# Optimization experiments

Hardware: AMD Instinct MI355X
Metric: run time of the kernel (lower is better)

Reference implementation:

```python
import jax, jax.numpy as jnp
import numpy as np

D_MODEL = 1024
N_HEADS = 16
D_K = D_MODEL // N_HEADS
B, S = 2, 2048


def setup_inputs() -> dict:
    key = jax.random.key(0)
    ks = jax.random.split(key, 11)
    s = 1.0 / np.sqrt(D_MODEL)
    return {
        "q": jax.random.normal(ks[0], (B, S, D_MODEL), jnp.float32),
        "k": jax.random.normal(ks[1], (B, S, D_MODEL), jnp.float32),
        "v": jax.random.normal(ks[2], (B, S, D_MODEL), jnp.float32),
        "Wq": jax.random.normal(ks[3], (D_MODEL, D_MODEL), jnp.float32) * s,
        "bq": jnp.zeros((D_MODEL,), jnp.float32),
        "Wk": jax.random.normal(ks[4], (D_MODEL, D_MODEL), jnp.float32) * s,
        "bk": jnp.zeros((D_MODEL,), jnp.float32),
        "Wv": jax.random.normal(ks[5], (D_MODEL, D_MODEL), jnp.float32) * s,
        "bv": jnp.zeros((D_MODEL,), jnp.float32),
        "Wo": jax.random.normal(ks[6], (D_MODEL, D_MODEL), jnp.float32) * s,
        "bo": jnp.zeros((D_MODEL,), jnp.float32),
    }


def reference(q, k, v, Wq, bq, Wk, bk, Wv, bv, Wo, bo):
    b = q.shape[0]
    # linear projections then split heads: [b, s, d] -> [b, h, s, d_k]
    def proj(x, W, bias):
        y = jnp.einsum('bsd,ed->bse', x, W) + bias  # torch Linear: x @ W.T + b
        return y.reshape(b, -1, N_HEADS, D_K).transpose(0, 2, 1, 3)

    qh, kh, vh = proj(q, Wq, bq), proj(k, Wk, bk), proj(v, Wv, bv)
    scores = jnp.einsum('bhqd,bhkd->bhqk', qh, kh) / np.sqrt(D_K)
    attn = jax.nn.softmax(scores, axis=-1)  # dropout: identity (eval mode)
    x = jnp.einsum('bhqk,bhkd->bhqd', attn, vh)
    x = x.transpose(0, 2, 1, 3).reshape(b, -1, D_MODEL)
    return jnp.einsum('bsd,ed->bse', x, Wo) + bo
```

## Files before the change

kernel.cpp:

```cpp
#include <hip/hip_runtime.h>
#include <math.h>
#include <stdint.h>

#define DM 1024
#define NH 16
#define DKH 64
#define BB 2
#define SS 2048
#define MM (BB*SS)

typedef __bf16 bf16;
typedef __bf16 bf16x8 __attribute__((ext_vector_type(8)));
typedef __bf16 bf16x4 __attribute__((ext_vector_type(4)));
typedef float f32x4 __attribute__((ext_vector_type(4)));

#define MFMA16(a,b,c) __builtin_amdgcn_mfma_f32_16x16x32_bf16((a),(b),(c),0,0,0)

#define SOFTMAX_C 12.0f
#define QSCALE 0.1803368801111204f

__device__ static inline void g2l16(const void* g, void* l) {
  __builtin_amdgcn_global_load_lds(
      (const __attribute__((address_space(1))) unsigned int*)g,
      (__attribute__((address_space(3))) unsigned int*)l, 16, 0, 0);
}

__global__ __launch_bounds__(256) void cvt_all(
    const float* __restrict__ q, const float* __restrict__ k, const float* __restrict__ v,
    const float* __restrict__ wq, const float* __restrict__ wk,
    const float* __restrict__ wv, const float* __restrict__ wo,
    bf16* __restrict__ Xq, bf16* __restrict__ Xk, bf16* __restrict__ Xv,
    bf16* __restrict__ Wqb, bf16* __restrict__ Wkb, bf16* __restrict__ Wvb,
    bf16* __restrict__ Wob)
{
  const long i = (long)blockIdx.x * 256 + threadIdx.x;
  const float* src; bf16* dst; long off;
  if (i < 3L * 524288L) {
    const int a = (int)(i / 524288L);
    off = (i % 524288L) * 8;
    src = (a == 0) ? q : (a == 1) ? k : v;
    dst = (a == 0) ? Xq : (a == 1) ? Xk : Xv;
  } else {
    const long j = i - 3L * 524288L;
    const int a = (int)(j / 131072L);
    off = (j % 131072L) * 8;
    src = (a == 0) ? wq : (a == 1) ? wk : (a == 2) ? wv : wo;
    dst = (a == 0) ? Wqb : (a == 1) ? Wkb : (a == 2) ? Wvb : Wob;
  }
  float4 f0 = *(const float4*)(src + off);
  float4 f1 = *(const float4*)(src + off + 4);
  bf16x8 o;
  o[0] = (bf16)f0.x; o[1] = (bf16)f0.y; o[2] = (bf16)f0.z; o[3] = (bf16)f0.w;
  o[4] = (bf16)f1.x; o[5] = (bf16)f1.y; o[6] = (bf16)f1.z; o[7] = (bf16)f1.w;
  *(bf16x8*)(dst + off) = o;
}

template<int BN, bool SWAP>
__device__ __forceinline__ void gemm_bt_body(
    const bf16* __restrict__ A, const bf16* __restrict__ W,
    const float* __restrict__ bias, void* __restrict__ Y, float scale, int ep)
{
  constexpr int NT = BN / 32;
  constexpr int PB = BN / 32;
  constexpr int SMEM = (BN == 128) ? 34816 : 24576;
  __shared__ __align__(16) char smem[SMEM];
  const int tid = threadIdx.x;
  const int lane = tid & 63, w = tid >> 6;
  const int ln15 = lane & 15, q4 = lane >> 4;
  const int m0 = blockIdx.x * 128;
  const int n0 = blockIdx.y * BN;
  const int mhalf = (w >> 1) * 64, nhalf = (w & 1) * (BN / 2);

  const bf16* gA[4]; const bf16* gB[PB];
  char* lA[4]; char* lB[PB];
  #pragma unroll
  for (int p = 0; p < 4; ++p) {
    const int n = p * 256 + tid;
    const int row = n >> 3, u = n & 7;
    const int g = u ^ (row & 7);
    gA[p] = A + (size_t)(m0 + row) * DM + g * 8;
    lA[p] = smem + n * 16;
  }
  #pragma unroll
  for (int p = 0; p < PB; ++p) {
    const int n = p * 256 + tid;
    const int row = n >> 3, u = n & 7;
    const int g = u ^ (row & 7);
    gB[p] = W + (size_t)(n0 + row) * DM + g * 8;
    lB[p] = smem + 16384 + n * 16;
  }

  int aoff[4][2], boff[NT][2];
  #pragma unroll
  for (int mt = 0; mt < 4; ++mt) {
    const int row = mhalf + mt * 16 + ln15;
    #pragma unroll
    for (int kc = 0; kc < 2; ++kc)
      aoff[mt][kc] = (row * 8 + ((kc * 4 + q4) ^ (row & 7))) * 16;
  }
  #pragma unroll
  for (int nt = 0; nt < NT; ++nt) {
    const int row = nhalf + nt * 16 + ln15;
    #pragma unroll
    for (int kc = 0; kc < 2; ++kc)
      boff[nt][kc] = 16384 + (row * 8 + ((kc * 4 + q4) ^ (row & 7))) * 16;
  }

  f32x4 acc[4][NT] = {};

  for (int kt = 0; kt < DM; kt += 64) {
    __syncthreads();
    #pragma unroll
    for (int p = 0; p < 4; ++p) g2l16(gA[p] + kt, lA[p]);
    #pragma unroll
    for (int p = 0; p < PB; ++p) g2l16(gB[p] + kt, lB[p]);
    asm volatile("s_waitcnt vmcnt(0)" ::: "memory");
    __syncthreads();
    #pragma unroll
    for (int kc = 0; kc < 2; ++kc) {
      bf16x8 af[4];
      #pragma unroll
      for (int mt = 0; mt < 4; ++mt) af[mt] = *(const bf16x8*)(smem + aoff[mt][kc]);
      #pragma unroll
      for (int nt = 0; nt < NT; ++nt) {
        bf16x8 bfr = *(const bf16x8*)(smem + boff[nt][kc]);
        #pragma unroll
        for (int mt = 0; mt < 4; ++mt)
          acc[mt][nt] = SWAP ? MFMA16(bfr, af[mt], acc[mt][nt])
                             : MFMA16(af[mt], bfr, acc[mt][nt]);
      }
    }
  }

  if (SWAP) {
    if (ep == 0) {
      #pragma unroll
      for (int nt = 0; nt < NT; ++nt) {
        const int col0 = n0 + nhalf + nt * 16 + q4 * 4;
        const float4 bi = *(const float4*)(bias + col0);
        #pragma unroll
        for (int mt = 0; mt < 4; ++mt) {
          const int row = m0 + mhalf + mt * 16 + ln15;
          float4 rr;
          rr.x = acc[mt][nt][0] + bi.x;
          rr.y = acc[mt][nt][1] + bi.y;
          rr.z = acc[mt][nt][2] + bi.z;
          rr.w = acc[mt][nt][3] + bi.w;
          *(float4*)((float*)Y + (size_t)row * DM + col0) = rr;
        }
      }
    } else {
      __syncthreads();
      #pragma unroll
      for (int nt = 0; nt < NT; ++nt) {
        const int colL = nhalf + nt * 16 + q4 * 4;
        const float4 bi = *(const float4*)(bias + n0 + colL);
        #pragma unroll
        for (int mt = 0; mt < 4; ++mt) {
          const int sL = mhalf + mt * 16 + ln15;
          bf16x4 pk;
          pk[0] = (bf16)((acc[mt][nt][0] + bi.x) * scale);
          pk[1] = (bf16)((acc[mt][nt][1] + bi.y) * scale);
          pk[2] = (bf16)((acc[mt][nt][2] + bi.z) * scale);
          pk[3] = (bf16)((acc[mt][nt][3] + bi.w) * scale);
          *(bf16x4*)(smem + sL * 272 + colL * 2) = pk;
        }
      }
      __syncthreads();
      const int lrow = tid >> 1, hs = tid & 1;
      const int b = m0 >> 11, s = (m0 & 2047) + lrow;
      const int h = (n0 >> 6) + hs;
      bf16* dq = (bf16*)Y + (((size_t)(b * NH + h) * SS + s) * DKH);
      #pragma unroll
      for (int i = 0; i < 8; ++i) {
        bf16x8 vv = *(const bf16x8*)(smem + lrow * 272 + hs * 128 + i * 16);
        *(bf16x8*)(dq + i * 8) = vv;
      }
    }
    return;
  }

  __syncthreads();
  #pragma unroll
  for (int nt = 0; nt < NT; ++nt) {
    const int col = nhalf + nt * 16 + ln15;
    const float bv = bias[n0 + col];
    #pragma unroll
    for (int mt = 0; mt < 4; ++mt) {
      const int s = mhalf + mt * 16 + q4 * 4;
      const int u = (s >> 3) ^ ln15;
      bf16x4 pk;
      #pragma unroll
      for (int r = 0; r < 4; ++r) pk[r] = (bf16)(acc[mt][nt][r] + bv);
      *(bf16x4*)(smem + col * 256 + u * 16 + (s & 7) * 2) = pk;
    }
  }
  __syncthreads();
  {
    const int col = tid >> 1, hs = tid & 1;
    const int gh = (n0 + col) >> 6, gdk = (n0 + col) & 63;
    const int bB = m0 >> 11;
    bf16* dstb = (bf16*)Y + ((size_t)(bB * NH + gh) * DKH + gdk) * SS
                 + (m0 & 2047) + hs * 64;
    #pragma unroll
    for (int i = 0; i < 8; ++i) {
      const int u = (hs * 8 + i) ^ (col & 15);
      bf16x8 vv = *(const bf16x8*)(smem + col * 256 + u * 16);
      *(bf16x8*)(dstb + i * 8) = vv;
    }
  }
}

__global__ __launch_bounds__(256) void gemm_qkv(
    const bf16* Xq, const bf16* Xk, const bf16* Xv,
    const bf16* Wq, const bf16* Wk, const bf16* Wv,
    const float* bq, const float* bk, const float* bv,
    bf16* qh, bf16* kh, bf16* vth)
{
  const int z = blockIdx.z;
  const bf16* A = (z == 0) ? Xq : (z == 1) ? Xk : Xv;
  const bf16* W = (z == 0) ? Wq : (z == 1) ? Wk : Wv;
  const float* bias = (z == 0) ? bq : (z == 1) ? bk : bv;
  bf16* Y = (z == 0) ? qh : (z == 1) ? kh : vth;
  const float scale = (z == 0) ? QSCALE : 1.0f;
  if (z < 2) gemm_bt_body<128, true >(A, W, bias, Y, scale, 1);
  else       gemm_bt_body<128, false>(A, W, bias, Y, scale, 2);
}

__global__ __launch_bounds__(256) void gemm_out(
    const bf16* A, const bf16* W, const float* bias, float* Y)
{
  gemm_bt_body<64, true>(A, W, bias, Y, 1.0f, 0);
}

__global__ __launch_bounds__(256) void attn_mfma(
    const bf16* __restrict__ Qh, const bf16* __restrict__ Kh,
    const bf16* __restrict__ Vth, bf16* __restrict__ Xout)
{
  __shared__ __align__(16) char smem[51200];
  const int tid = threadIdx.x, lane = tid & 63, w = tid >> 6;
  const int ln15 = lane & 15, q4 = lane >> 4;
  const int bh = blockIdx.y, b = bh >> 4, h = bh & 15;
  const int q0 = blockIdx.x * 128 + w * 32;
  const bf16* Qb = Qh + (size_t)bh * SS * DKH;
  const bf16* Kb = Kh + (size_t)bh * SS * DKH;
  const bf16* Vb = Vth + (size_t)bh * SS * DKH;

  bf16x8 qf[2][2];
  #pragma unroll
  for (int qt = 0; qt < 2; ++qt)
    #pragma unroll
    for (int kc = 0; kc < 2; ++kc)
      qf[qt][kc] = *(const bf16x8*)(Qb + (size_t)(q0 + qt * 16 + ln15) * DKH + kc * 32 + q4 * 8);

  bf16x8 ones_frag;
  #pragma unroll
  for (int j = 0; j < 8; ++j) ones_frag[j] = (bf16)1.0f;

  const bf16* gK[2]; const bf16* gV[2];
  char* lK[2]; char* lV[2];
  #pragma unroll
  for (int p = 0; p < 2; ++p) {
    const int n = p * 256 + tid;
    const int row = n >> 3, u = n & 7;
    const int g = u ^ (row & 7);
    gK[p] = Kb + (size_t)row * DKH + g * 8;
    gV[p] = Vb + (size_t)row * SS + g * 8;
    lK[p] = smem + n * 16;
    lV[p] = smem + 8192 + n * 16;
  }
  char* Pl = smem + 32768 + w * 4608;

  int koff[4][2], voff[4][2], pst[4][2], pld[2][2];
  #pragma unroll
  for (int nt = 0; nt < 4; ++nt) {
    const int rowi = nt * 16 + ln15;
    #pragma unroll
    for (int kc = 0; kc < 2; ++kc) {
      koff[nt][kc] = (rowi * 8 + ((kc * 4 + q4) ^ (rowi & 7))) * 16;
      voff[nt][kc] = 8192 + (rowi * 8 + ((kc * 4 + q4) ^ (rowi & 7))) * 16;
    }
  }
  #pragma unroll
  for (int k4 = 0; k4 < 4; ++k4)
    #pragma unroll
    for (int qt = 0; qt < 2; ++qt)
      pst[k4][qt] = (qt * 16 + ln15) * 144 + (k4 * 16 + q4 * 4) * 2;
  #pragma unroll
  for (int qt = 0; qt < 2; ++qt)
    #pragma unroll
    for (int kc = 0; kc < 2; ++kc)
      pld[qt][kc] = (qt * 16 + ln15) * 144 + kc * 64 + q4 * 16;

  f32x4 Oa[4][2] = {};
  f32x4 Ol[2] = {};

  #pragma unroll
  for (int p = 0; p < 2; ++p) {
    g2l16(gK[p], lK[p]); g2l16(gV[p], lV[p]);
    gK[p] += 64 * DKH; gV[p] += 64;
  }

  for (int kt = 0; kt < SS / 64; ++kt) {
    const int cur = (kt & 1) << 14;
    asm volatile("s_waitcnt vmcnt(0)" ::: "memory");
    __syncthreads();
    if (kt < SS / 64 - 1) {
      const int nxt = (~kt & 1) << 14;
      #pragma unroll
      for (int p = 0; p < 2; ++p) {
        g2l16(gK[p], lK[p] + nxt); g2l16(gV[p], lV[p] + nxt);
        gK[p] += 64 * DKH; gV[p] += 64;
      }
    }

    f32x4 St[4][2];
    #pragma unroll
    for (int k4 = 0; k4 < 4; ++k4)
      #pragma unroll
      for (int qt = 0; qt < 2; ++qt)
        St[k4][qt] = (f32x4){-SOFTMAX_C, -SOFTMAX_C, -SOFTMAX_C, -SOFTMAX_C};
    #pragma unroll
    for (int kc = 0; kc < 2; ++kc) {
      #pragma unroll
      for (int k4 = 0; k4 < 4; ++k4) {
        bf16x8 kf = *(const bf16x8*)(smem + cur + koff[k4][kc]);
        #pragma unroll
        for (int qt = 0; qt < 2; ++qt)
          St[k4][qt] = MFMA16(kf, qf[qt][kc], St[k4][qt]);
      }
    }

    #pragma unroll
    for (int k4 = 0; k4 < 4; ++k4)
      #pragma unroll
      for (int qt = 0; qt < 2; ++qt) {
        bf16x4 pk;
        #pragma unroll
        for (int r = 0; r < 4; ++r)
          pk[r] = (bf16)__builtin_amdgcn_exp2f(St[k4][qt][r]);
        *(bf16x4*)(Pl + pst[k4][qt]) = pk;
      }
    asm volatile("s_waitcnt lgkmcnt(0)" ::: "memory");

    #pragma unroll
    for (int kc = 0; kc < 2; ++kc) {
      bf16x8 pf[2];
      #pragma unroll
      for (int qt = 0; qt < 2; ++qt) pf[qt] = *(const bf16x8*)(Pl + pld[qt][kc]);
      #pragma unroll
      for (int dt = 0; dt < 4; ++dt) {
        bf16x8 vf = *(const bf16x8*)(smem + cur + voff[dt][kc]);
        #pragma unroll
        for (int qt = 0; qt < 2; ++qt)
          Oa[dt][qt] = MFMA16(vf, pf[qt], Oa[dt][qt]);
      }
      #pragma unroll
      for (int qt = 0; qt < 2; ++qt)
        Ol[qt] = MFMA16(ones_frag, pf[qt], Ol[qt]);
    }
  }

  #pragma unroll
  for (int qt = 0; qt < 2; ++qt) {
    const float inv = 1.f / Ol[qt][0];
    const int srow = q0 + qt * 16 + ln15;
    bf16* dst = Xout + (size_t)(b * SS + srow) * DM + h * DKH + q4 * 4;
    #pragma unroll
    for (int dt = 0; dt < 4; ++dt) {
      bf16x4 o4;
      #pragma unroll
      for (int r = 0; r < 4; ++r) o4[r] = (bf16)(Oa[dt][qt][r] * inv);
      *(bf16x4*)(dst + dt * 16) = o4;
    }
  }
}

extern "C" void kernel_launch(void* const* d_in, const int* in_sizes, int n_in,
                              void* d_out, int out_size, void* d_ws, size_t ws_size,
                              hipStream_t stream)
{
  const float* q  = (const float*)d_in[0];
  const float* k  = (const float*)d_in[1];
  const float* v  = (const float*)d_in[2];
  const float* Wq = (const float*)d_in[3];
  const float* bq = (const float*)d_in[4];
  const float* Wk = (const float*)d_in[5];
  const float* bk = (const float*)d_in[6];
  const float* Wv = (const float*)d_in[7];
  const float* bv = (const float*)d_in[8];
  const float* Wo = (const float*)d_in[9];
  const float* bo = (const float*)d_in[10];
  float* out = (float*)d_out;

  char* ws = (char*)d_ws;
  const size_t MB = 1u << 20;
  bf16* Xq  = (bf16*)(ws + 0);
  bf16* Xk  = (bf16*)(ws + 8 * MB);
  bf16* Xv  = (bf16*)(ws + 16 * MB);
  bf16* Wqb = (bf16*)(ws + 24 * MB);
  bf16* Wkb = (bf16*)(ws + 26 * MB);
  bf16* Wvb = (bf16*)(ws + 28 * MB);
  bf16* Wob = (bf16*)(ws + 30 * MB);
  bf16* qh  = (bf16*)(ws + 32 * MB);
  bf16* kh  = (bf16*)(ws + 40 * MB);
  bf16* vth = (bf16*)(ws + 48 * MB);
  bf16* xh  = Xq;

  cvt_all<<<8192, 256, 0, stream>>>(q, k, v, Wq, Wk, Wv, Wo,
                                    Xq, Xk, Xv, Wqb, Wkb, Wvb, Wob);

  gemm_qkv<<<dim3(32, 8, 3), 256, 0, stream>>>(Xq, Xk, Xv, Wqb, Wkb, Wvb,
                                               bq, bk, bv, qh, kh, vth);

  attn_mfma<<<dim3(16, 32), 256, 0, stream>>>(qh, kh, vth, xh);

  gemm_out<<<dim3(32, 16), 256, 0, stream>>>(xh, Wob, bo, out);
}
```

Before: 229.0 us.

## Double-buffer W tiles in LDS and prefetch A fragments directly to registers

Rewrites the GEMM main loop so the weight tile is double-buffered in LDS, with the next tile loaded while the current one is consumed. The A operand is no longer staged through LDS; each lane loads its MFMA fragments straight from global memory into registers, one iteration ahead. This aims to hide global load latency and cut LDS traffic and barriers, at the cost of more registers and less coalesced A loads. The launch bounds also request three blocks per CU.

```diff
diff --git a/kernel.cpp b/kernel.cpp
--- a/kernel.cpp
+++ b/kernel.cpp
@@ -62,7 +62,8 @@
 {
   constexpr int NT = BN / 32;
   constexpr int PB = BN / 32;
-  constexpr int SMEM = (BN == 128) ? 34816 : 24576;
+  constexpr int BUFB = BN * 128;
+  constexpr int SMEM = (BN == 128) ? 34816 : 16384;
   __shared__ __align__(16) char smem[SMEM];
   const int tid = threadIdx.x;
   const int lane = tid & 63, w = tid >> 6;
@@ -71,63 +72,66 @@
   const int n0 = blockIdx.y * BN;
   const int mhalf = (w >> 1) * 64, nhalf = (w & 1) * (BN / 2);
 
-  const bf16* gA[4]; const bf16* gB[PB];
-  char* lA[4]; char* lB[PB];
-  #pragma unroll
-  for (int p = 0; p < 4; ++p) {
-    const int n = p * 256 + tid;
-    const int row = n >> 3, u = n & 7;
-    const int g = u ^ (row & 7);
-    gA[p] = A + (size_t)(m0 + row) * DM + g * 8;
-    lA[p] = smem + n * 16;
-  }
+  const bf16* gB[PB]; int lBoff[PB];
   #pragma unroll
   for (int p = 0; p < PB; ++p) {
     const int n = p * 256 + tid;
     const int row = n >> 3, u = n & 7;
     const int g = u ^ (row & 7);
     gB[p] = W + (size_t)(n0 + row) * DM + g * 8;
-    lB[p] = smem + 16384 + n * 16;
-  }
-
-  int aoff[4][2], boff[NT][2];
-  #pragma unroll
-  for (int mt = 0; mt < 4; ++mt) {
-    const int row = mhalf + mt * 16 + ln15;
-    #pragma unroll
-    for (int kc = 0; kc < 2; ++kc)
-      aoff[mt][kc] = (row * 8 + ((kc * 4 + q4) ^ (row & 7))) * 16;
-  }
+    lBoff[p] = n * 16;
+  }
+
+  const bf16* gA4[4];
+  #pragma unroll
+  for (int mt = 0; mt < 4; ++mt)
+    gA4[mt] = A + (size_t)(m0 + mhalf + mt * 16 + ln15) * DM + q4 * 8;
+
+  int boff[NT][2];
   #pragma unroll
   for (int nt = 0; nt < NT; ++nt) {
     const int row = nhalf + nt * 16 + ln15;
     #pragma unroll
     for (int kc = 0; kc < 2; ++kc)
-      boff[nt][kc] = 16384 + (row * 8 + ((kc * 4 + q4) ^ (row & 7))) * 16;
+      boff[nt][kc] = (row * 8 + ((kc * 4 + q4) ^ (row & 7))) * 16;
   }
 
   f32x4 acc[4][NT] = {};
-
-  for (int kt = 0; kt < DM; kt += 64) {
-    __syncthreads();
-    #pragma unroll
-    for (int p = 0; p < 4; ++p) g2l16(gA[p] + kt, lA[p]);
-    #pragma unroll
-    for (int p = 0; p < PB; ++p) g2l16(gB[p] + kt, lB[p]);
+  bf16x8 af[2][4][2];
+
+  #pragma unroll
+  for (int p = 0; p < PB; ++p) g2l16(gB[p], smem + lBoff[p]);
+  #pragma unroll
+  for (int mt = 0; mt < 4; ++mt)
+    #pragma unroll
+    for (int kc = 0; kc < 2; ++kc)
+      af[0][mt][kc] = *(const bf16x8*)(gA4[mt] + kc * 32);
+
+  #pragma unroll
+  for (int it = 0; it < DM / 64; ++it) {
+    const int cur = it & 1;
     asm volatile("s_waitcnt vmcnt(0)" ::: "memory");
     __syncthreads();
+    if (it + 1 < DM / 64) {
+      const int nb = (cur ^ 1) * BUFB;
+      #pragma unroll
+      for (int p = 0; p < PB; ++p) g2l16(gB[p] + (it + 1) * 64, smem + nb + lBoff[p]);
+      #pragma unroll
+      for (int mt = 0; mt < 4; ++mt)
+        #pragma unroll
+        for (int kc = 0; kc < 2; ++kc)
+          af[cur ^ 1][mt][kc] = *(const bf16x8*)(gA4[mt] + (it + 1) * 64 + kc * 32);
+    }
+    const int cb = cur * BUFB;
     #pragma unroll
     for (int kc = 0; kc < 2; ++kc) {
-      bf16x8 af[4];
-      #pragma unroll
-      for (int mt = 0; mt < 4; ++mt) af[mt] = *(const bf16x8*)(smem + aoff[mt][kc]);
       #pragma unroll
       for (int nt = 0; nt < NT; ++nt) {
-        bf16x8 bfr = *(const bf16x8*)(smem + boff[nt][kc]);
+        bf16x8 bfr = *(const bf16x8*)(smem + cb + boff[nt][kc]);
         #pragma unroll
         for (int mt = 0; mt < 4; ++mt)
-          acc[mt][nt] = SWAP ? MFMA16(bfr, af[mt], acc[mt][nt])
-                             : MFMA16(af[mt], bfr, acc[mt][nt]);
+          acc[mt][nt] = SWAP ? MFMA16(bfr, af[cur][mt][kc], acc[mt][nt])
+                             : MFMA16(af[cur][mt][kc], bfr, acc[mt][nt]);
       }
     }
   }
@@ -211,7 +215,7 @@
   }
 }
 
-__global__ __launch_bounds__(256) void gemm_qkv(
+__global__ __launch_bounds__(256, 3) void gemm_qkv(
     const bf16* Xq, const bf16* Xk, const bf16* Xv,
     const bf16* Wq, const bf16* Wk, const bf16* Wv,
     const float* bq, const float* bk, const float* bv,
@@ -227,7 +231,7 @@
   else       gemm_bt_body<128, false>(A, W, bias, Y, scale, 2);
 }
 
-__global__ __launch_bounds__(256) void gemm_out(
+__global__ __launch_bounds__(256, 3) void gemm_out(
     const bf16* A, const bf16* W, const float* bias, float* Y)
 {
   gemm_bt_body<64, true>(A, W, bias, Y, 1.0f, 0);
```

Result: slower. 291.6 us (+27.3%).
